# Kernel optimization log

Hardware: AMD Instinct MI355X
Metric: run time of the kernel (lower is better)

Reference implementation:

```python
import jax, jax.numpy as jnp
import numpy as np

B, N, C, H = 2, 2048, 1024, 16
D = C // H  # head_dim = 64
EPS = 1e-6


def _rope_freqs(n, d):
    inv_freq = 1.0 / (10000.0 ** (np.arange(0, d // 2, dtype=np.float32) * 2.0 / d))
    ang = np.arange(n, dtype=np.float32)[:, None] * inv_freq[None, :]  # [N, D/2]
    ang = np.concatenate([ang, ang], axis=-1)  # [N, D] (chunk-in-half convention)
    cos = jnp.asarray(np.cos(ang))[None, None]  # [1,1,N,D]
    sin = jnp.asarray(np.sin(ang))[None, None]
    return cos, sin


def setup_inputs() -> dict:
    key = jax.random.key(0)
    k1, k2, k3 = jax.random.split(key, 3)
    x = jax.random.normal(k1, (B, N, C), dtype=jnp.float32)
    w_qkv = jax.random.normal(k2, (3 * C, C), dtype=jnp.float32) * (C ** -0.5)
    w_proj = jax.random.normal(k3, (C, C), dtype=jnp.float32) * (C ** -0.5)
    b_proj = jnp.zeros((C,), dtype=jnp.float32)
    freqs_cos, freqs_sin = _rope_freqs(N, D)
    return {"x": x, "w_qkv": w_qkv, "w_proj": w_proj, "b_proj": b_proj,
            "freqs_cos": freqs_cos, "freqs_sin": freqs_sin}


def _layernorm(t):
    # affine-free LayerNorm over the last (head_dim) axis
    mu = jnp.mean(t, axis=-1, keepdims=True)
    var = jnp.var(t, axis=-1, keepdims=True)
    return (t - mu) * jax.lax.rsqrt(var + EPS)


def _rotate_half(t):
    t1, t2 = jnp.split(t, 2, axis=-1)
    return jnp.concatenate([-t2, t1], axis=-1)


def reference(x, w_qkv, w_proj, b_proj, freqs_cos, freqs_sin):
    b, n, c = x.shape
    qkv = jnp.einsum('bnc,kc->bnk', x, w_qkv)  # [B,N,3C]
    qkv = qkv.reshape(b, n, 3, H, D).transpose(2, 0, 3, 1, 4)  # [3,B,H,N,D]
    q, k, v = qkv[0], qkv[1], qkv[2]
    q = _layernorm(q)
    k = _layernorm(k)
    q = q * freqs_cos + _rotate_half(q) * freqs_sin
    k = k * freqs_cos + _rotate_half(k) * freqs_sin
    scale = D ** -0.5
    scores = jnp.einsum('bhqd,bhkd->bhqk', q, k) * scale  # [B,H,N,N]
    attn = jax.nn.softmax(scores, axis=-1)
    out = jnp.einsum('bhqk,bhkd->bhqd', attn, v)  # [B,H,N,D]
    out = out.transpose(0, 2, 1, 3).reshape(b, n, c)
    return jnp.einsum('bnc,oc->bno', out, w_proj) + b_proj
```

## Files before the change

### kernel.cpp

```cpp
#include <hip/hip_runtime.h>
#include <hip/hip_bf16.h>


typedef __bf16 bf16x8 __attribute__((ext_vector_type(8)));
typedef float f32x4 __attribute__((ext_vector_type(4)));
typedef float f32x16 __attribute__((ext_vector_type(16)));
typedef unsigned short us8 __attribute__((ext_vector_type(8)));
typedef unsigned short us4 __attribute__((ext_vector_type(4)));

static __device__ __forceinline__ unsigned short f2b(float f) {
  __hip_bfloat16 h = __float2bfloat16(f);
  return __builtin_bit_cast(unsigned short, h);
}
static __device__ __forceinline__ float b2f(unsigned short u) {
  __hip_bfloat16 h = __builtin_bit_cast(__hip_bfloat16, u);
  return __bfloat162float(h);
}

#if __has_builtin(__builtin_amdgcn_exp2f)
static __device__ __forceinline__ float fast_exp2(float x) { return __builtin_amdgcn_exp2f(x); }
#else
static __device__ __forceinline__ float fast_exp2(float x) { return exp2f(x); }
#endif

static __device__ __forceinline__ void async_copy16(void* lds, const void* g) {
  __builtin_amdgcn_global_load_lds(
      (const __attribute__((address_space(1))) void*)g,
      (__attribute__((address_space(3))) void*)lds, 16, 0, 0);
}

static __device__ __forceinline__ unsigned cvt_pk_bf16(float lo, float hi) {
  unsigned r;
  asm("v_cvt_pk_bf16_f32 %0, %1, %2" : "=v"(r) : "v"(lo), "v"(hi));
  return r;
}
static __device__ __forceinline__ void swap32(unsigned& x, unsigned& y) {
  asm("v_permlane32_swap_b32 %0, %1" : "+v"(x), "+v"(y));
}
static __device__ __forceinline__ float max3f(float a, float b, float c) {
  float d;
  asm("v_max3_f32 %0, %1, %2, %3" : "=v"(d) : "v"(a), "v"(b), "v"(c));
  return d;
}
static __device__ __forceinline__ float vmax16(const f32x16& v) {
  float a = max3f(v[0], v[1], v[2]);
  float b = max3f(v[3], v[4], v[5]);
  float c = max3f(v[6], v[7], v[8]);
  float d = max3f(v[9], v[10], v[11]);
  float e = max3f(v[12], v[13], v[14]);
  float x = max3f(a, b, c);
  float y = max3f(d, e, v[15]);
  return fmaxf(x, y);
}

__global__ __launch_bounds__(256) void cvt_bf16(
    const float* __restrict__ in, unsigned short* __restrict__ out, int n8) {
  int i = blockIdx.x * 256 + threadIdx.x;
  if (i >= n8) return;
  const float4* p = reinterpret_cast<const float4*>(in) + (size_t)i * 2;
  float4 a = p[0], b = p[1];
  us8 v;
  v[0] = f2b(a.x); v[1] = f2b(a.y); v[2] = f2b(a.z); v[3] = f2b(a.w);
  v[4] = f2b(b.x); v[5] = f2b(b.y); v[6] = f2b(b.z); v[7] = f2b(b.w);
  reinterpret_cast<us8*>(out)[i] = v;
}

__global__ __launch_bounds__(256, 2) void gemm_qkv(
    const unsigned short* __restrict__ A,
    const unsigned short* __restrict__ Bw,
    const float* __restrict__ fcos, const float* __restrict__ fsin,
    unsigned short* __restrict__ qo, unsigned short* __restrict__ ko,
    unsigned short* __restrict__ vt)
{
  __shared__ unsigned short a_sh[128 * 64];
  __shared__ unsigned short b_sh[128 * 64];
  const int tid = threadIdx.x;
  const int lane = tid & 63;
  const int w = tid >> 6;
  const int wr = w >> 1, wc = w & 1;
  const int l15 = lane & 15, l4 = lane >> 4;
  const int m0 = blockIdx.y * 128;
  const int n0 = blockIdx.x * 128;
  const int r8 = lane >> 3, c8 = lane & 7;
  const int K = 1024;

  f32x4 acc[4][4] = {};

  for (int k0 = 0; k0 < K; k0 += 64) {
#pragma unroll
    for (int p = 0; p < 8; ++p) {
      int s = p * 4 + w;
      if (s < 16) {
        int row = s * 8 + r8;
        async_copy16(&a_sh[s * 512],
                     &A[(size_t)(m0 + row) * K + k0 + ((c8 ^ (row & 7)) << 3)]);
      } else {
        int s2 = s - 16;
        int row = s2 * 8 + r8;
        async_copy16(&b_sh[s2 * 512],
                     &Bw[(size_t)(n0 + row) * K + k0 + ((c8 ^ (row & 7)) << 3)]);
      }
    }
    __syncthreads();
#pragma unroll
    for (int kk = 0; kk < 2; ++kk) {
      bf16x8 af[4], bfr[4];
#pragma unroll
      for (int mf = 0; mf < 4; ++mf) {
        int r = wr * 64 + mf * 16 + l15;
        af[mf] = *reinterpret_cast<const bf16x8*>(
            &a_sh[r * 64 + (((kk * 4 + l4) ^ (r & 7)) << 3)]);
      }
#pragma unroll
      for (int nf = 0; nf < 4; ++nf) {
        int r = wc * 64 + nf * 16 + l15;
        bfr[nf] = *reinterpret_cast<const bf16x8*>(
            &b_sh[r * 64 + (((kk * 4 + l4) ^ (r & 7)) << 3)]);
      }
#pragma unroll
      for (int mf = 0; mf < 4; ++mf)
#pragma unroll
        for (int nf = 0; nf < 4; ++nf)
          acc[mf][nf] = __builtin_amdgcn_mfma_f32_16x16x32_bf16(af[mf], bfr[nf], acc[mf][nf], 0, 0, 0);
    }
    __syncthreads();
  }

  const int colbase = n0 + wc * 64;
  const int three = colbase >> 10;
  const int hh = (colbase >> 6) & 15;
  const int b_ = m0 >> 11;
  const int nbase = (m0 & 2047) + wr * 64;
  unsigned short* ep = ((w < 2) ? a_sh : b_sh) + (w & 1) * 4096;
  const int cch = lane & 7, rb2 = lane >> 3;

  if (three < 2) {
    const float sc = three ? 1.f : 0.18033688011112042f;
#pragma unroll
    for (int mf = 0; mf < 4; ++mf) {
#pragma unroll
      for (int j = 0; j < 4; ++j) {
        float a0 = acc[mf][0][j], a1 = acc[mf][1][j];
        float a2 = acc[mf][2][j], a3 = acc[mf][3][j];
        float s1 = (a0 + a1) + (a2 + a3);
        float s2 = (a0 * a0 + a1 * a1) + (a2 * a2 + a3 * a3);
#pragma unroll
        for (int off = 8; off; off >>= 1) {
          s1 += __shfl_xor(s1, off);
          s2 += __shfl_xor(s2, off);
        }
        float mu = s1 * (1.f / 64.f);
        float inv = rsqrtf(s2 * (1.f / 64.f) - mu * mu + 1e-6f);
        int rloc = mf * 16 + l4 * 4 + j;
        int n = nbase + rloc;
        const float* cp = &fcos[(size_t)n * 64];
        const float* sp = &fsin[(size_t)n * 64];
#pragma unroll
        for (int nf = 0; nf < 4; ++nf) {
          int d = nf * 16 + l15;
          float t = (acc[mf][nf][j] - mu) * inv;
          float tp = (acc[mf][nf ^ 2][j] - mu) * inv;
          float r = sc * (t * cp[d] + ((nf < 2) ? -tp : tp) * sp[d]);
          ep[rloc * 64 + ((((d >> 3) ^ (rloc & 7)) << 3) | (d & 7))] = f2b(r);
        }
      }
    }
    unsigned short* dst =
        (three ? ko : qo) + (size_t)(b_ * 16 + hh) * 2048 * 64;
#pragma unroll
    for (int i = 0; i < 8; ++i) {
      int row = i * 8 + rb2;
      us8 vd = *reinterpret_cast<const us8*>(
          &ep[row * 64 + ((cch ^ (row & 7)) << 3)]);
      *reinterpret_cast<us8*>(&dst[(size_t)(nbase + row) * 64 + cch * 8]) = vd;
    }
  } else {
#pragma unroll
    for (int mf = 0; mf < 4; ++mf)
#pragma unroll
      for (int nf = 0; nf < 4; ++nf) {
        int d = nf * 16 + l15;
#pragma unroll
        for (int j = 0; j < 4; ++j) {
          int nl = mf * 16 + l4 * 4 + j;
          ep[d * 64 + ((((nl >> 3) ^ (d & 7)) << 3) | (nl & 7))] =
              f2b(acc[mf][nf][j]);
        }
      }
    unsigned short* dst = vt + (size_t)(b_ * 16 + hh) * 64 * 2048;
#pragma unroll
    for (int i = 0; i < 8; ++i) {
      int d = i * 8 + rb2;
      us8 vd = *reinterpret_cast<const us8*>(
          &ep[d * 64 + ((cch ^ (d & 7)) << 3)]);
      *reinterpret_cast<us8*>(&dst[(size_t)d * 2048 + nbase + cch * 8]) = vd;
    }
  }
}

__global__ __launch_bounds__(256, 2) void gemm_proj(
    const unsigned short* __restrict__ A, const unsigned short* __restrict__ Bw,
    const float* __restrict__ bias, float* __restrict__ Cout,
    int M, int Nn, int K) {
  __shared__ unsigned short a_sh[128 * 64];
  __shared__ unsigned short b_sh[128 * 64];
  const int tid = threadIdx.x;
  const int lane = tid & 63;
  const int w = tid >> 6;
  const int wr = w >> 1, wc = w & 1;
  const int l15 = lane & 15, l4 = lane >> 4;
  const int m0 = blockIdx.y * 128;
  const int n0 = blockIdx.x * 128;
  const int r8 = lane >> 3, c8 = lane & 7;

  f32x4 acc[4][4] = {};

  for (int k0 = 0; k0 < K; k0 += 64) {
#pragma unroll
    for (int p = 0; p < 8; ++p) {
      int s = p * 4 + w;
      if (s < 16) {
        int row = s * 8 + r8;
        async_copy16(&a_sh[s * 512],
                     &A[(size_t)(m0 + row) * K + k0 + ((c8 ^ (row & 7)) << 3)]);
      } else {
        int s2 = s - 16;
        int row = s2 * 8 + r8;
        async_copy16(&b_sh[s2 * 512],
                     &Bw[(size_t)(n0 + row) * K + k0 + ((c8 ^ (row & 7)) << 3)]);
      }
    }
    __syncthreads();
#pragma unroll
    for (int kk = 0; kk < 2; ++kk) {
      bf16x8 af[4], bfr[4];
#pragma unroll
      for (int mf = 0; mf < 4; ++mf) {
        int r = wr * 64 + mf * 16 + l15;
        af[mf] = *reinterpret_cast<const bf16x8*>(
            &a_sh[r * 64 + (((kk * 4 + l4) ^ (r & 7)) << 3)]);
      }
#pragma unroll
      for (int nf = 0; nf < 4; ++nf) {
        int r = wc * 64 + nf * 16 + l15;
        bfr[nf] = *reinterpret_cast<const bf16x8*>(
            &b_sh[r * 64 + (((kk * 4 + l4) ^ (r & 7)) << 3)]);
      }
#pragma unroll
      for (int mf = 0; mf < 4; ++mf)
#pragma unroll
        for (int nf = 0; nf < 4; ++nf)
          acc[mf][nf] = __builtin_amdgcn_mfma_f32_16x16x32_bf16(af[mf], bfr[nf], acc[mf][nf], 0, 0, 0);
    }
    __syncthreads();
  }
#pragma unroll
  for (int mf = 0; mf < 4; ++mf)
#pragma unroll
    for (int nf = 0; nf < 4; ++nf) {
      int col = n0 + wc * 64 + nf * 16 + l15;
#pragma unroll
      for (int j = 0; j < 4; ++j) {
        int row = m0 + wr * 64 + mf * 16 + l4 * 4 + j;
        Cout[(size_t)row * Nn + col] = acc[mf][nf][j] + bias[col];
      }
    }
}

__global__ __launch_bounds__(256, 2) void attn_kern(
    const unsigned short* __restrict__ Q,
    const unsigned short* __restrict__ Kk,
    const unsigned short* __restrict__ Vt,
    unsigned short* __restrict__ O)
{
  __shared__ unsigned short k_sh[2][128 * 64];
  __shared__ unsigned short v_sh[2][64 * 128];
  const int tid = threadIdx.x;
  const int lane = tid & 63;
  const int w = tid >> 6;
  const int l31 = lane & 31;
  const int H = lane >> 5;
  const int bid = blockIdx.x;
  const int wid = (bid & 7) * 64 + (bid >> 3);
  const int qt = wid & 15;
  const int bh = wid >> 4;
  const int h = bh & 15, b = bh >> 4;
  const unsigned short* qb = Q + (size_t)bh * 2048 * 64;
  const unsigned short* kb = Kk + (size_t)bh * 2048 * 64;
  const unsigned short* vb = Vt + (size_t)bh * 64 * 2048;
  const int tok = qt * 128 + w * 32 + l31;

  bf16x8 qf[4];
#pragma unroll
  for (int c = 0; c < 4; ++c)
    qf[c] = *reinterpret_cast<const bf16x8*>(&qb[(size_t)tok * 64 + c * 16 + H * 8]);

  f32x16 oT[2] = {};
  float mr = -1e30f, lr = 0.f;

  const int r8 = lane >> 3, cc8 = lane & 7;
  const int r4 = lane >> 4, cc16 = lane & 15;
#define ATTN_STAGE(KT, BUF)                                                           \
  {                                                                                   \
    _Pragma("unroll") for (int p = 0; p < 8; ++p) {                                   \
      int sseg = p * 4 + w;                                                           \
      if (sseg < 16) {                                                                \
        int row = sseg * 8 + r8;                                                      \
        async_copy16(&k_sh[BUF][sseg * 512],                                          \
                     &kb[(size_t)((KT) * 128 + row) * 64 + ((cc8 ^ (row & 7)) << 3)]);   \
      } else {                                                                        \
        int s2 = sseg - 16;                                                           \
        int row = s2 * 4 + r4;                                                        \
        async_copy16(&v_sh[BUF][s2 * 512],                                            \
                     &vb[(size_t)row * 2048 + (KT) * 128 + ((cc16 ^ (row & 7)) << 3)]);  \
      }                                                                               \
    }                                                                                 \
  }

  ATTN_STAGE(0, 0);
  __syncthreads();

  for (int kt = 0; kt < 16; ++kt) {
    const int cur = kt & 1;
    if (kt < 15) ATTN_STAGE(kt + 1, cur ^ 1);

    f32x16 sT[4] = {};
    __builtin_amdgcn_s_setprio(1);
#pragma unroll
    for (int c = 0; c < 4; ++c) {
      int ch0 = 2 * c + H;
#pragma unroll
      for (int t = 0; t < 4; ++t) {
        int r = t * 32 + l31;
        bf16x8 ka = *reinterpret_cast<const bf16x8*>(
            &k_sh[cur][r * 64 + (((ch0) ^ (r & 7)) << 3)]);
        sT[t] = __builtin_amdgcn_mfma_f32_32x32x16_bf16(ka, qf[c], sT[t], 0, 0, 0);
      }
    }
    __builtin_amdgcn_s_setprio(0);
    float tmax = fmaxf(fmaxf(vmax16(sT[0]), vmax16(sT[1])),
                       fmaxf(vmax16(sT[2]), vmax16(sT[3])));
    tmax = fmaxf(tmax, __shfl_xor(tmax, 32));
    if (__any(tmax > mr + 8.f)) {
      float mn = fmaxf(mr, tmax);
      float corr = fast_exp2(mr - mn);
      mr = mn;
      lr *= corr;
#pragma unroll
      for (int r = 0; r < 16; ++r) { oT[0][r] *= corr; oT[1][r] *= corr; }
    }
    float tsum = 0.f;
#pragma unroll
    for (int t = 0; t < 4; ++t)
#pragma unroll
      for (int r = 0; r < 16; ++r) {
        float p = fast_exp2(sT[t][r] - mr);
        sT[t][r] = p;
        tsum += p;
      }
    tsum += __shfl_xor(tsum, 32);
    lr += tsum;

    bf16x8 pB[8];
#pragma unroll
    for (int t = 0; t < 4; ++t)
#pragma unroll
      for (int half = 0; half < 2; ++half) {
        const int base = 8 * half;
        unsigned x0 = cvt_pk_bf16(sT[t][base + 0], sT[t][base + 1]);
        unsigned x1 = cvt_pk_bf16(sT[t][base + 2], sT[t][base + 3]);
        unsigned y0 = cvt_pk_bf16(sT[t][base + 4], sT[t][base + 5]);
        unsigned y1 = cvt_pk_bf16(sT[t][base + 6], sT[t][base + 7]);
        swap32(x0, y0);
        swap32(x1, y1);
        int4 packed = {(int)x0, (int)x1, (int)y0, (int)y1};
        pB[2 * t + half] = __builtin_bit_cast(bf16x8, packed);
      }
    __builtin_amdgcn_s_setprio(1);
#pragma unroll
    for (int dt = 0; dt < 2; ++dt) {
      int r = dt * 32 + l31;
#pragma unroll
      for (int mi = 0; mi < 8; ++mi) {
        int ch = (mi * 2 + H) ^ (r & 7);
        bf16x8 va = *reinterpret_cast<const bf16x8*>(&v_sh[cur][r * 128 + (ch << 3)]);
        oT[dt] = __builtin_amdgcn_mfma_f32_32x32x16_bf16(va, pB[mi], oT[dt], 0, 0, 0);
      }
    }
    __builtin_amdgcn_s_setprio(0);
    __syncthreads();
  }
  float invl = 1.f / lr;
#pragma unroll
  for (int dt = 0; dt < 2; ++dt)
#pragma unroll
    for (int rb = 0; rb < 4; ++rb) {
      us4 ov;
#pragma unroll
      for (int j = 0; j < 4; ++j) ov[j] = f2b(oT[dt][rb * 4 + j] * invl);
      *reinterpret_cast<us4*>(
          &O[((size_t)b * 2048 + tok) * 1024 + h * 64 + 32 * dt + 8 * rb + 4 * H]) = ov;
    }
#undef ATTN_STAGE
}

extern "C" void kernel_launch(void* const* d_in, const int* in_sizes, int n_in,
                              void* d_out, int out_size, void* d_ws, size_t ws_size,
                              hipStream_t stream) {
  (void)in_sizes; (void)n_in; (void)out_size; (void)ws_size;
  const float* x      = (const float*)d_in[0];
  const float* w_qkv  = (const float*)d_in[1];
  const float* w_proj = (const float*)d_in[2];
  const float* b_proj = (const float*)d_in[3];
  const float* fcos   = (const float*)d_in[4];
  const float* fsin   = (const float*)d_in[5];
  float* out = (float*)d_out;
  char* ws = (char*)d_ws;

  unsigned short* x_bf     = (unsigned short*)(ws + 0);
  unsigned short* wqkv_bf  = (unsigned short*)(ws + 8388608);
  unsigned short* wproj_bf = (unsigned short*)(ws + 14680064);
  unsigned short* q_bf     = (unsigned short*)(ws + 16777216);
  unsigned short* k_bf     = (unsigned short*)(ws + 25165824);
  unsigned short* vt_bf    = (unsigned short*)(ws + 33554432);
  unsigned short* ao_bf    = (unsigned short*)(ws + 41943040);

  cvt_bf16<<<2048, 256, 0, stream>>>(x, x_bf, 4096 * 1024 / 8);
  cvt_bf16<<<1536, 256, 0, stream>>>(w_qkv, wqkv_bf, 3072 * 1024 / 8);
  cvt_bf16<<<512, 256, 0, stream>>>(w_proj, wproj_bf, 1024 * 1024 / 8);
  gemm_qkv<<<dim3(24, 32), 256, 0, stream>>>(x_bf, wqkv_bf, fcos, fsin,
                                             q_bf, k_bf, vt_bf);
  attn_kern<<<512, 256, 0, stream>>>(q_bf, k_bf, vt_bf, ao_bf);
  gemm_proj<<<dim3(8, 32), 256, 0, stream>>>(ao_bf, wproj_bf, b_proj, out,
                                             4096, 1024, 1024);
}
```

Before: 124.4 us.

## Double-buffer GEMM K-loop and shrink attention KV tile for higher occupancy

Both GEMM kernels now double-buffer their shared-memory A/B tiles, so the next K-slice is prefetched while MFMAs run on the current one, instead of a load-sync-compute loop. The attention kernel halves its KV tile from 128 to 64 keys, which halves its shared-memory footprint, and raises the launch-bound occupancy hint from 2 to 3. It also drops the s_setprio hints. The GEMMs now use twice the shared memory, and attention does twice as many iterations, each with a barrier and an online-softmax update.

After: 133.6 us. +7.4%, slower.

```diff
diff --git a/kernel.cpp b/kernel.cpp
--- a/kernel.cpp
+++ b/kernel.cpp
@@ -65,6 +65,44 @@
   reinterpret_cast<us8*>(out)[i] = v;
 }
 
+#define GEMM_STAGE(APTR, BPTR, KOFF, BUF)                                        \
+  {                                                                              \
+    _Pragma("unroll") for (int p = 0; p < 8; ++p) {                              \
+      int s = p * 4 + w;                                                         \
+      if (s < 16) {                                                              \
+        int row = s * 8 + r8;                                                    \
+        async_copy16(&a_sh[BUF][s * 512],                                        \
+                     &APTR[(size_t)(m0 + row) * K + (KOFF) + ((c8 ^ (row & 7)) << 3)]); \
+      } else {                                                                   \
+        int s2 = s - 16;                                                         \
+        int row = s2 * 8 + r8;                                                   \
+        async_copy16(&b_sh[BUF][s2 * 512],                                       \
+                     &BPTR[(size_t)(n0 + row) * K + (KOFF) + ((c8 ^ (row & 7)) << 3)]); \
+      }                                                                          \
+    }                                                                            \
+  }
+
+#define GEMM_COMPUTE(BUF)                                                        \
+  {                                                                              \
+    _Pragma("unroll") for (int kk = 0; kk < 2; ++kk) {                           \
+      bf16x8 af[4], bfr[4];                                                      \
+      _Pragma("unroll") for (int mf = 0; mf < 4; ++mf) {                         \
+        int r = wr * 64 + mf * 16 + l15;                                         \
+        af[mf] = *reinterpret_cast<const bf16x8*>(                               \
+            &a_sh[BUF][r * 64 + (((kk * 4 + l4) ^ (r & 7)) << 3)]);              \
+      }                                                                          \
+      _Pragma("unroll") for (int nf = 0; nf < 4; ++nf) {                         \
+        int r = wc * 64 + nf * 16 + l15;                                         \
+        bfr[nf] = *reinterpret_cast<const bf16x8*>(                              \
+            &b_sh[BUF][r * 64 + (((kk * 4 + l4) ^ (r & 7)) << 3)]);              \
+      }                                                                          \
+      _Pragma("unroll") for (int mf = 0; mf < 4; ++mf)                           \
+          _Pragma("unroll") for (int nf = 0; nf < 4; ++nf)                       \
+              acc[mf][nf] = __builtin_amdgcn_mfma_f32_16x16x32_bf16(             \
+                  af[mf], bfr[nf], acc[mf][nf], 0, 0, 0);                        \
+    }                                                                            \
+  }
+
 __global__ __launch_bounds__(256, 2) void gemm_qkv(
     const unsigned short* __restrict__ A,
     const unsigned short* __restrict__ Bw,
@@ -72,8 +110,8 @@
     unsigned short* __restrict__ qo, unsigned short* __restrict__ ko,
     unsigned short* __restrict__ vt)
 {
-  __shared__ unsigned short a_sh[128 * 64];
-  __shared__ unsigned short b_sh[128 * 64];
+  __shared__ unsigned short a_sh[2][128 * 64];
+  __shared__ unsigned short b_sh[2][128 * 64];
   const int tid = threadIdx.x;
   const int lane = tid & 63;
   const int w = tid >> 6;
@@ -86,43 +124,13 @@
 
   f32x4 acc[4][4] = {};
 
-  for (int k0 = 0; k0 < K; k0 += 64) {
-#pragma unroll
-    for (int p = 0; p < 8; ++p) {
-      int s = p * 4 + w;
-      if (s < 16) {
-        int row = s * 8 + r8;
-        async_copy16(&a_sh[s * 512],
-                     &A[(size_t)(m0 + row) * K + k0 + ((c8 ^ (row & 7)) << 3)]);
-      } else {
-        int s2 = s - 16;
-        int row = s2 * 8 + r8;
-        async_copy16(&b_sh[s2 * 512],
-                     &Bw[(size_t)(n0 + row) * K + k0 + ((c8 ^ (row & 7)) << 3)]);
-      }
-    }
-    __syncthreads();
-#pragma unroll
-    for (int kk = 0; kk < 2; ++kk) {
-      bf16x8 af[4], bfr[4];
-#pragma unroll
-      for (int mf = 0; mf < 4; ++mf) {
-        int r = wr * 64 + mf * 16 + l15;
-        af[mf] = *reinterpret_cast<const bf16x8*>(
-            &a_sh[r * 64 + (((kk * 4 + l4) ^ (r & 7)) << 3)]);
-      }
-#pragma unroll
-      for (int nf = 0; nf < 4; ++nf) {
-        int r = wc * 64 + nf * 16 + l15;
-        bfr[nf] = *reinterpret_cast<const bf16x8*>(
-            &b_sh[r * 64 + (((kk * 4 + l4) ^ (r & 7)) << 3)]);
-      }
-#pragma unroll
-      for (int mf = 0; mf < 4; ++mf)
-#pragma unroll
-        for (int nf = 0; nf < 4; ++nf)
-          acc[mf][nf] = __builtin_amdgcn_mfma_f32_16x16x32_bf16(af[mf], bfr[nf], acc[mf][nf], 0, 0, 0);
-    }
+  GEMM_STAGE(A, Bw, 0, 0);
+  __syncthreads();
+#pragma unroll 2
+  for (int t = 0; t < 16; ++t) {
+    const int cur = t & 1;
+    if (t < 15) GEMM_STAGE(A, Bw, (t + 1) * 64, cur ^ 1);
+    GEMM_COMPUTE(cur);
     __syncthreads();
   }
 
@@ -131,7 +139,7 @@
   const int hh = (colbase >> 6) & 15;
   const int b_ = m0 >> 11;
   const int nbase = (m0 & 2047) + wr * 64;
-  unsigned short* ep = ((w < 2) ? a_sh : b_sh) + (w & 1) * 4096;
+  unsigned short* ep = &a_sh[0][0] + w * 4096;
   const int cch = lane & 7, rb2 = lane >> 3;
 
   if (three < 2) {
@@ -158,9 +166,9 @@
 #pragma unroll
         for (int nf = 0; nf < 4; ++nf) {
           int d = nf * 16 + l15;
-          float t = (acc[mf][nf][j] - mu) * inv;
+          float tt = (acc[mf][nf][j] - mu) * inv;
           float tp = (acc[mf][nf ^ 2][j] - mu) * inv;
-          float r = sc * (t * cp[d] + ((nf < 2) ? -tp : tp) * sp[d]);
+          float r = sc * (tt * cp[d] + ((nf < 2) ? -tp : tp) * sp[d]);
           ep[rloc * 64 + ((((d >> 3) ^ (rloc & 7)) << 3) | (d & 7))] = f2b(r);
         }
       }
@@ -202,8 +210,8 @@
     const unsigned short* __restrict__ A, const unsigned short* __restrict__ Bw,
     const float* __restrict__ bias, float* __restrict__ Cout,
     int M, int Nn, int K) {
-  __shared__ unsigned short a_sh[128 * 64];
-  __shared__ unsigned short b_sh[128 * 64];
+  __shared__ unsigned short a_sh[2][128 * 64];
+  __shared__ unsigned short b_sh[2][128 * 64];
   const int tid = threadIdx.x;
   const int lane = tid & 63;
   const int w = tid >> 6;
@@ -215,43 +223,14 @@
 
   f32x4 acc[4][4] = {};
 
-  for (int k0 = 0; k0 < K; k0 += 64) {
-#pragma unroll
-    for (int p = 0; p < 8; ++p) {
-      int s = p * 4 + w;
-      if (s < 16) {
-        int row = s * 8 + r8;
-        async_copy16(&a_sh[s * 512],
-                     &A[(size_t)(m0 + row) * K + k0 + ((c8 ^ (row & 7)) << 3)]);
-      } else {
-        int s2 = s - 16;
-        int row = s2 * 8 + r8;
-        async_copy16(&b_sh[s2 * 512],
-                     &Bw[(size_t)(n0 + row) * K + k0 + ((c8 ^ (row & 7)) << 3)]);
-      }
-    }
-    __syncthreads();
-#pragma unroll
-    for (int kk = 0; kk < 2; ++kk) {
-      bf16x8 af[4], bfr[4];
-#pragma unroll
-      for (int mf = 0; mf < 4; ++mf) {
-        int r = wr * 64 + mf * 16 + l15;
-        af[mf] = *reinterpret_cast<const bf16x8*>(
-            &a_sh[r * 64 + (((kk * 4 + l4) ^ (r & 7)) << 3)]);
-      }
-#pragma unroll
-      for (int nf = 0; nf < 4; ++nf) {
-        int r = wc * 64 + nf * 16 + l15;
-        bfr[nf] = *reinterpret_cast<const bf16x8*>(
-            &b_sh[r * 64 + (((kk * 4 + l4) ^ (r & 7)) << 3)]);
-      }
-#pragma unroll
-      for (int mf = 0; mf < 4; ++mf)
-#pragma unroll
-        for (int nf = 0; nf < 4; ++nf)
-          acc[mf][nf] = __builtin_amdgcn_mfma_f32_16x16x32_bf16(af[mf], bfr[nf], acc[mf][nf], 0, 0, 0);
-    }
+  GEMM_STAGE(A, Bw, 0, 0);
+  __syncthreads();
+  const int nt = K >> 6;
+#pragma unroll 2
+  for (int t = 0; t < nt; ++t) {
+    const int cur = t & 1;
+    if (t + 1 < nt) GEMM_STAGE(A, Bw, (t + 1) * 64, cur ^ 1);
+    GEMM_COMPUTE(cur);
     __syncthreads();
   }
 #pragma unroll
@@ -267,14 +246,14 @@
     }
 }
 
-__global__ __launch_bounds__(256, 2) void attn_kern(
+__global__ __launch_bounds__(256, 3) void attn_kern(
     const unsigned short* __restrict__ Q,
     const unsigned short* __restrict__ Kk,
     const unsigned short* __restrict__ Vt,
     unsigned short* __restrict__ O)
 {
-  __shared__ unsigned short k_sh[2][128 * 64];
-  __shared__ unsigned short v_sh[2][64 * 128];
+  __shared__ unsigned short k_sh[2][64 * 64];
+  __shared__ unsigned short v_sh[2][64 * 64];
   const int tid = threadIdx.x;
   const int lane = tid & 63;
   const int w = tid >> 6;
@@ -299,47 +278,42 @@
   float mr = -1e30f, lr = 0.f;
 
   const int r8 = lane >> 3, cc8 = lane & 7;
-  const int r4 = lane >> 4, cc16 = lane & 15;
-#define ATTN_STAGE(KT, BUF)                                                           \
-  {                                                                                   \
-    _Pragma("unroll") for (int p = 0; p < 8; ++p) {                                   \
-      int sseg = p * 4 + w;                                                           \
-      if (sseg < 16) {                                                                \
-        int row = sseg * 8 + r8;                                                      \
-        async_copy16(&k_sh[BUF][sseg * 512],                                          \
-                     &kb[(size_t)((KT) * 128 + row) * 64 + ((cc8 ^ (row & 7)) << 3)]);   \
-      } else {                                                                        \
-        int s2 = sseg - 16;                                                           \
-        int row = s2 * 4 + r4;                                                        \
-        async_copy16(&v_sh[BUF][s2 * 512],                                            \
-                     &vb[(size_t)row * 2048 + (KT) * 128 + ((cc16 ^ (row & 7)) << 3)]);  \
-      }                                                                               \
-    }                                                                                 \
+#define ATTN_STAGE(KT, BUF)                                                        \
+  {                                                                                \
+    _Pragma("unroll") for (int p = 0; p < 4; ++p) {                                \
+      int sseg = p * 4 + w;                                                        \
+      if (sseg < 8) {                                                              \
+        int row = sseg * 8 + r8;                                                   \
+        async_copy16(&k_sh[BUF][sseg * 512],                                       \
+                     &kb[(size_t)((KT) * 64 + row) * 64 + ((cc8 ^ (row & 7)) << 3)]); \
+      } else {                                                                     \
+        int row = (sseg - 8) * 8 + r8;                                             \
+        async_copy16(&v_sh[BUF][(sseg - 8) * 512],                                 \
+                     &vb[(size_t)row * 2048 + (KT) * 64 + ((cc8 ^ (row & 7)) << 3)]); \
+      }                                                                            \
+    }                                                                              \
   }
 
   ATTN_STAGE(0, 0);
   __syncthreads();
 
-  for (int kt = 0; kt < 16; ++kt) {
+  for (int kt = 0; kt < 32; ++kt) {
     const int cur = kt & 1;
-    if (kt < 15) ATTN_STAGE(kt + 1, cur ^ 1);
-
-    f32x16 sT[4] = {};
-    __builtin_amdgcn_s_setprio(1);
+    if (kt < 31) ATTN_STAGE(kt + 1, cur ^ 1);
+
+    f32x16 sT[2] = {};
 #pragma unroll
     for (int c = 0; c < 4; ++c) {
       int ch0 = 2 * c + H;
 #pragma unroll
-      for (int t = 0; t < 4; ++t) {
+      for (int t = 0; t < 2; ++t) {
         int r = t * 32 + l31;
         bf16x8 ka = *reinterpret_cast<const bf16x8*>(
-            &k_sh[cur][r * 64 + (((ch0) ^ (r & 7)) << 3)]);
+            &k_sh[cur][r * 64 + ((ch0 ^ (r & 7)) << 3)]);
         sT[t] = __builtin_amdgcn_mfma_f32_32x32x16_bf16(ka, qf[c], sT[t], 0, 0, 0);
       }
     }
-    __builtin_amdgcn_s_setprio(0);
-    float tmax = fmaxf(fmaxf(vmax16(sT[0]), vmax16(sT[1])),
-                       fmaxf(vmax16(sT[2]), vmax16(sT[3])));
+    float tmax = fmaxf(vmax16(sT[0]), vmax16(sT[1]));
     tmax = fmaxf(tmax, __shfl_xor(tmax, 32));
     if (__any(tmax > mr + 8.f)) {
       float mn = fmaxf(mr, tmax);
@@ -351,7 +325,7 @@
     }
     float tsum = 0.f;
 #pragma unroll
-    for (int t = 0; t < 4; ++t)
+    for (int t = 0; t < 2; ++t)
 #pragma unroll
       for (int r = 0; r < 16; ++r) {
         float p = fast_exp2(sT[t][r] - mr);
@@ -361,9 +335,9 @@
     tsum += __shfl_xor(tsum, 32);
     lr += tsum;
 
-    bf16x8 pB[8];
-#pragma unroll
-    for (int t = 0; t < 4; ++t)
+    bf16x8 pB[4];
+#pragma unroll
+    for (int t = 0; t < 2; ++t)
 #pragma unroll
       for (int half = 0; half < 2; ++half) {
         const int base = 8 * half;
@@ -376,18 +350,16 @@
         int4 packed = {(int)x0, (int)x1, (int)y0, (int)y1};
         pB[2 * t + half] = __builtin_bit_cast(bf16x8, packed);
       }
-    __builtin_amdgcn_s_setprio(1);
 #pragma unroll
     for (int dt = 0; dt < 2; ++dt) {
       int r = dt * 32 + l31;
 #pragma unroll
-      for (int mi = 0; mi < 8; ++mi) {
+      for (int mi = 0; mi < 4; ++mi) {
         int ch = (mi * 2 + H) ^ (r & 7);
-        bf16x8 va = *reinterpret_cast<const bf16x8*>(&v_sh[cur][r * 128 + (ch << 3)]);
+        bf16x8 va = *reinterpret_cast<const bf16x8*>(&v_sh[cur][r * 64 + (ch << 3)]);
         oT[dt] = __builtin_amdgcn_mfma_f32_32x32x16_bf16(va, pB[mi], oT[dt], 0, 0, 0);
       }
     }
-    __builtin_amdgcn_s_setprio(0);
     __syncthreads();
   }
   float invl = 1.f / lr;
```

## Split attention over two KV halves with a separate merge kernel

Applied to the files above, without the earlier changes.

The attention kernel now splits each query tile's key range into two halves processed by separate blocks. Each block writes an unnormalised bf16 partial output plus per-row max and sum statistics, and a new merge kernel combines the halves with log-sum-exp weights. KV tiles shrink to 64 keys, shared memory is halved, launch bounds allow 4 blocks per CU, and the s_setprio hints are removed. The goal is more parallelism and occupancy (1024 blocks instead of 512), at the cost of an extra kernel launch, extra global traffic for partials, and extra bf16 rounding of the unnormalised partials.

Result: slower. 129.1 us (+3.8%).

```diff
diff --git a/kernel.cpp b/kernel.cpp
--- a/kernel.cpp
+++ b/kernel.cpp
@@ -158,9 +158,9 @@
 #pragma unroll
         for (int nf = 0; nf < 4; ++nf) {
           int d = nf * 16 + l15;
-          float t = (acc[mf][nf][j] - mu) * inv;
+          float tt = (acc[mf][nf][j] - mu) * inv;
           float tp = (acc[mf][nf ^ 2][j] - mu) * inv;
-          float r = sc * (t * cp[d] + ((nf < 2) ? -tp : tp) * sp[d]);
+          float r = sc * (tt * cp[d] + ((nf < 2) ? -tp : tp) * sp[d]);
           ep[rloc * 64 + ((((d >> 3) ^ (rloc & 7)) << 3) | (d & 7))] = f2b(r);
         }
       }
@@ -267,28 +267,31 @@
     }
 }
 
-__global__ __launch_bounds__(256, 2) void attn_kern(
+__global__ __launch_bounds__(256, 4) void attn_kern(
     const unsigned short* __restrict__ Q,
     const unsigned short* __restrict__ Kk,
     const unsigned short* __restrict__ Vt,
-    unsigned short* __restrict__ O)
+    unsigned short* __restrict__ po,
+    float* __restrict__ stats)
 {
-  __shared__ unsigned short k_sh[2][128 * 64];
-  __shared__ unsigned short v_sh[2][64 * 128];
+  __shared__ unsigned short k_sh[2][64 * 64];
+  __shared__ unsigned short v_sh[2][64 * 64];
   const int tid = threadIdx.x;
   const int lane = tid & 63;
   const int w = tid >> 6;
   const int l31 = lane & 31;
   const int H = lane >> 5;
   const int bid = blockIdx.x;
-  const int wid = (bid & 7) * 64 + (bid >> 3);
-  const int qt = wid & 15;
-  const int bh = wid >> 4;
+  const int wid = (bid & 7) * 128 + (bid >> 3);
+  const int split = wid & 1;
+  const int qt = (wid >> 1) & 15;
+  const int bh = wid >> 5;
   const int h = bh & 15, b = bh >> 4;
   const unsigned short* qb = Q + (size_t)bh * 2048 * 64;
   const unsigned short* kb = Kk + (size_t)bh * 2048 * 64;
   const unsigned short* vb = Vt + (size_t)bh * 64 * 2048;
   const int tok = qt * 128 + w * 32 + l31;
+  const int kt0 = split * 16;
 
   bf16x8 qf[4];
 #pragma unroll
@@ -299,47 +302,42 @@
   float mr = -1e30f, lr = 0.f;
 
   const int r8 = lane >> 3, cc8 = lane & 7;
-  const int r4 = lane >> 4, cc16 = lane & 15;
-#define ATTN_STAGE(KT, BUF)                                                           \
-  {                                                                                   \
-    _Pragma("unroll") for (int p = 0; p < 8; ++p) {                                   \
-      int sseg = p * 4 + w;                                                           \
-      if (sseg < 16) {                                                                \
-        int row = sseg * 8 + r8;                                                      \
-        async_copy16(&k_sh[BUF][sseg * 512],                                          \
-                     &kb[(size_t)((KT) * 128 + row) * 64 + ((cc8 ^ (row & 7)) << 3)]);   \
-      } else {                                                                        \
-        int s2 = sseg - 16;                                                           \
-        int row = s2 * 4 + r4;                                                        \
-        async_copy16(&v_sh[BUF][s2 * 512],                                            \
-                     &vb[(size_t)row * 2048 + (KT) * 128 + ((cc16 ^ (row & 7)) << 3)]);  \
-      }                                                                               \
-    }                                                                                 \
-  }
-
-  ATTN_STAGE(0, 0);
+#define ATTN_STAGE(KT, BUF)                                                        \
+  {                                                                                \
+    _Pragma("unroll") for (int p = 0; p < 4; ++p) {                                \
+      int sseg = p * 4 + w;                                                        \
+      if (sseg < 8) {                                                              \
+        int row = sseg * 8 + r8;                                                   \
+        async_copy16(&k_sh[BUF][sseg * 512],                                       \
+                     &kb[(size_t)((KT) * 64 + row) * 64 + ((cc8 ^ (row & 7)) << 3)]); \
+      } else {                                                                     \
+        int row = (sseg - 8) * 8 + r8;                                             \
+        async_copy16(&v_sh[BUF][(sseg - 8) * 512],                                 \
+                     &vb[(size_t)row * 2048 + (KT) * 64 + ((cc8 ^ (row & 7)) << 3)]); \
+      }                                                                            \
+    }                                                                              \
+  }
+
+  ATTN_STAGE(kt0, 0);
   __syncthreads();
 
   for (int kt = 0; kt < 16; ++kt) {
     const int cur = kt & 1;
-    if (kt < 15) ATTN_STAGE(kt + 1, cur ^ 1);
-
-    f32x16 sT[4] = {};
-    __builtin_amdgcn_s_setprio(1);
+    if (kt < 15) ATTN_STAGE(kt0 + kt + 1, cur ^ 1);
+
+    f32x16 sT[2] = {};
 #pragma unroll
     for (int c = 0; c < 4; ++c) {
       int ch0 = 2 * c + H;
 #pragma unroll
-      for (int t = 0; t < 4; ++t) {
+      for (int t = 0; t < 2; ++t) {
         int r = t * 32 + l31;
         bf16x8 ka = *reinterpret_cast<const bf16x8*>(
-            &k_sh[cur][r * 64 + (((ch0) ^ (r & 7)) << 3)]);
+            &k_sh[cur][r * 64 + ((ch0 ^ (r & 7)) << 3)]);
         sT[t] = __builtin_amdgcn_mfma_f32_32x32x16_bf16(ka, qf[c], sT[t], 0, 0, 0);
       }
     }
-    __builtin_amdgcn_s_setprio(0);
-    float tmax = fmaxf(fmaxf(vmax16(sT[0]), vmax16(sT[1])),
-                       fmaxf(vmax16(sT[2]), vmax16(sT[3])));
+    float tmax = fmaxf(vmax16(sT[0]), vmax16(sT[1]));
     tmax = fmaxf(tmax, __shfl_xor(tmax, 32));
     if (__any(tmax > mr + 8.f)) {
       float mn = fmaxf(mr, tmax);
@@ -351,7 +349,7 @@
     }
     float tsum = 0.f;
 #pragma unroll
-    for (int t = 0; t < 4; ++t)
+    for (int t = 0; t < 2; ++t)
 #pragma unroll
       for (int r = 0; r < 16; ++r) {
         float p = fast_exp2(sT[t][r] - mr);
@@ -361,9 +359,9 @@
     tsum += __shfl_xor(tsum, 32);
     lr += tsum;
 
-    bf16x8 pB[8];
-#pragma unroll
-    for (int t = 0; t < 4; ++t)
+    bf16x8 pB[4];
+#pragma unroll
+    for (int t = 0; t < 2; ++t)
 #pragma unroll
       for (int half = 0; half < 2; ++half) {
         const int base = 8 * half;
@@ -376,32 +374,60 @@
         int4 packed = {(int)x0, (int)x1, (int)y0, (int)y1};
         pB[2 * t + half] = __builtin_bit_cast(bf16x8, packed);
       }
-    __builtin_amdgcn_s_setprio(1);
 #pragma unroll
     for (int dt = 0; dt < 2; ++dt) {
       int r = dt * 32 + l31;
 #pragma unroll
-      for (int mi = 0; mi < 8; ++mi) {
+      for (int mi = 0; mi < 4; ++mi) {
         int ch = (mi * 2 + H) ^ (r & 7);
-        bf16x8 va = *reinterpret_cast<const bf16x8*>(&v_sh[cur][r * 128 + (ch << 3)]);
+        bf16x8 va = *reinterpret_cast<const bf16x8*>(&v_sh[cur][r * 64 + (ch << 3)]);
         oT[dt] = __builtin_amdgcn_mfma_f32_32x32x16_bf16(va, pB[mi], oT[dt], 0, 0, 0);
       }
     }
-    __builtin_amdgcn_s_setprio(0);
     __syncthreads();
   }
-  float invl = 1.f / lr;
+  if (H == 0) {
+    float2 st = {mr, lr};
+    *reinterpret_cast<float2*>(
+        &stats[(((size_t)split * 32 + bh) * 2048 + tok) * 2]) = st;
+  }
+  unsigned short* pd = po + (size_t)split * 4096 * 1024;
 #pragma unroll
   for (int dt = 0; dt < 2; ++dt)
 #pragma unroll
     for (int rb = 0; rb < 4; ++rb) {
       us4 ov;
 #pragma unroll
-      for (int j = 0; j < 4; ++j) ov[j] = f2b(oT[dt][rb * 4 + j] * invl);
+      for (int j = 0; j < 4; ++j) ov[j] = f2b(oT[dt][rb * 4 + j]);
       *reinterpret_cast<us4*>(
-          &O[((size_t)b * 2048 + tok) * 1024 + h * 64 + 32 * dt + 8 * rb + 4 * H]) = ov;
+          &pd[((size_t)b * 2048 + tok) * 1024 + h * 64 + 32 * dt + 8 * rb + 4 * H]) = ov;
     }
 #undef ATTN_STAGE
+}
+
+__global__ __launch_bounds__(256) void attn_merge(
+    const unsigned short* __restrict__ po,
+    const float* __restrict__ stats,
+    unsigned short* __restrict__ ao)
+{
+  int i = blockIdx.x * 256 + threadIdx.x;
+  int row = i >> 8;
+  int c4 = (i & 255) << 2;
+  int b = row >> 11, tok = row & 2047, h = c4 >> 6;
+  int bh = b * 16 + h;
+  float2 s0 = *reinterpret_cast<const float2*>(&stats[((size_t)bh * 2048 + tok) * 2]);
+  float2 s1 = *reinterpret_cast<const float2*>(
+      &stats[(((size_t)32 + bh) * 2048 + tok) * 2]);
+  float M = fmaxf(s0.x, s1.x);
+  float w0 = fast_exp2(s0.x - M), w1 = fast_exp2(s1.x - M);
+  float inv = 1.f / (s0.y * w0 + s1.y * w1);
+  w0 *= inv; w1 *= inv;
+  us4 a = *reinterpret_cast<const us4*>(&po[(size_t)i * 4]);
+  us4 c = *reinterpret_cast<const us4*>(&po[(size_t)4096 * 1024 + i * 4]);
+  us4 o;
+#pragma unroll
+  for (int j = 0; j < 4; ++j) o[j] = f2b(b2f(a[j]) * w0 + b2f(c[j]) * w1);
+  *reinterpret_cast<us4*>(&ao[(size_t)i * 4]) = o;
 }
 
 extern "C" void kernel_launch(void* const* d_in, const int* in_sizes, int n_in,
@@ -424,13 +450,16 @@
   unsigned short* k_bf     = (unsigned short*)(ws + 25165824);
   unsigned short* vt_bf    = (unsigned short*)(ws + 33554432);
   unsigned short* ao_bf    = (unsigned short*)(ws + 41943040);
+  unsigned short* po_bf    = (unsigned short*)(ws + 50331648);
+  float*          st_f     = (float*)(ws + 67108864);
 
   cvt_bf16<<<2048, 256, 0, stream>>>(x, x_bf, 4096 * 1024 / 8);
   cvt_bf16<<<1536, 256, 0, stream>>>(w_qkv, wqkv_bf, 3072 * 1024 / 8);
   cvt_bf16<<<512, 256, 0, stream>>>(w_proj, wproj_bf, 1024 * 1024 / 8);
   gemm_qkv<<<dim3(24, 32), 256, 0, stream>>>(x_bf, wqkv_bf, fcos, fsin,
                                              q_bf, k_bf, vt_bf);
-  attn_kern<<<512, 256, 0, stream>>>(q_bf, k_bf, vt_bf, ao_bf);
+  attn_kern<<<1024, 256, 0, stream>>>(q_bf, k_bf, vt_bf, po_bf, st_f);
+  attn_merge<<<4096, 256, 0, stream>>>(po_bf, st_f, ao_bf);
   gemm_proj<<<dim3(8, 32), 256, 0, stream>>>(ao_bf, wproj_bf, b_proj, out,
                                              4096, 1024, 1024);
 }
```
